# Kernel tuning notes

Hardware: AMD Instinct MI355X
Metric: run time of the kernel (lower is better)

The kernel has to match this reference:

```python
import jax, jax.numpy as jnp
import numpy as np

H = 8              # n_heads
N_PER_GRAPH = 64   # nodes per graph (equal-sized graphs)


def setup_inputs() -> dict:
    key = jax.random.key(0)
    ks = jax.random.split(key, 5)
    total, D = 65536, 512
    x = jax.random.normal(ks[0], (total, D), dtype=jnp.float32)
    batch = jnp.arange(total, dtype=jnp.int64) // N_PER_GRAPH  # sorted graph ids
    s = 1.0 / np.sqrt(D).astype(np.float32)
    # nn.MultiheadAttention packed in-proj (xavier-ish uniform) + zero bias
    in_proj_w = jax.random.uniform(ks[1], (3 * D, D), jnp.float32, -s, s)
    in_proj_b = jnp.zeros((3 * D,), jnp.float32)
    out_proj_w = jax.random.uniform(ks[2], (D, D), jnp.float32, -s, s)
    out_proj_b = jnp.zeros((D,), jnp.float32)
    gate_w = jax.random.uniform(ks[3], (1, D), jnp.float32, -s, s)
    gate_b = jnp.zeros((1,), jnp.float32)
    return {"x": x, "batch": batch, "in_proj_w": in_proj_w, "in_proj_b": in_proj_b,
            "out_proj_w": out_proj_w, "out_proj_b": out_proj_b,
            "gate_w": gate_w, "gate_b": gate_b}


def reference(x, batch, in_proj_w, in_proj_b, out_proj_w, out_proj_b, gate_w, gate_b):
    total, D = x.shape
    G = total // N_PER_GRAPH
    hd = D // H
    xg = x.reshape(G, N_PER_GRAPH, D)                       # [G, N, D]
    # packed qkv projection (torch: x @ in_proj_w.T + in_proj_b)
    qkv = jnp.einsum('gnd,ed->gne', xg, in_proj_w) + in_proj_b
    q, k, v = jnp.split(qkv, 3, axis=-1)
    def to_heads(t):
        return t.reshape(G, N_PER_GRAPH, H, hd).transpose(0, 2, 1, 3)  # [G, H, N, hd]
    q, k, v = to_heads(q), to_heads(k), to_heads(v)
    scores = jnp.einsum('ghnd,ghmd->ghnm', q, k) * (1.0 / np.sqrt(hd))
    attn = jax.nn.softmax(scores, axis=-1)
    ctx = jnp.einsum('ghnm,ghmd->ghnd', attn, v)
    ctx = ctx.transpose(0, 2, 1, 3).reshape(G, N_PER_GRAPH, D)
    attn_out = jnp.einsum('gnd,ed->gne', ctx, out_proj_w) + out_proj_b  # [G, N, D]
    gates = jax.nn.sigmoid(jnp.einsum('gnd,od->gno', attn_out, gate_w) + gate_b)
    return (attn_out * gates).sum(axis=1)                   # [G, D]
```

## Files before the change

### kernel.cpp

```cpp
#include <hip/hip_runtime.h>
#include <stdint.h>


typedef __attribute__((ext_vector_type(8))) short short8;
typedef __attribute__((ext_vector_type(4))) float f32x4;

#define D_ 512

#define WQKV_OFF   0u
#define WO_OFF     1572864u
#define UPART_OFF  2097152u
#define U_OFF      2129920u
#define C0_OFF     2131968u

__device__ __forceinline__ unsigned short f2bf(float f) {
    union { float f; unsigned int u; } t; t.f = f;
    unsigned int u = t.u;
    return (unsigned short)((u + 0x7FFFu + ((u >> 16) & 1u)) >> 16);
}
__device__ __forceinline__ unsigned pack2(float a, float b) {
    return (unsigned)f2bf(a) | ((unsigned)f2bf(b) << 16);
}
__device__ __forceinline__ float blo(unsigned v) {
    union { unsigned u; float f; } t; t.u = v << 16; return t.f;
}
__device__ __forceinline__ float bhi(unsigned v) {
    union { unsigned u; float f; } t; t.u = v & 0xFFFF0000u; return t.f;
}

__global__ __launch_bounds__(256)
void convert_and_u(const float* __restrict__ wqkv, const float* __restrict__ wo,
                   const float* __restrict__ gw,
                   unsigned short* __restrict__ wbf, float* __restrict__ upart) {
    const int b = blockIdx.x;
    const int t = threadIdx.x;
    if (b < 1024) {
        const int i4 = b * 256 + t;
        float4 v;
        if (i4 < 196608) v = *(const float4*)(wqkv + (size_t)i4 * 4);
        else             v = *(const float4*)(wo   + (size_t)(i4 - 196608) * 4);
        uint2 p; p.x = pack2(v.x, v.y); p.y = pack2(v.z, v.w);
        *(uint2*)(wbf + (size_t)i4 * 4) = p;
    } else {
        const int bb = b - 1024;
        float a0 = 0.f, a1 = 0.f;
        #pragma unroll 4
        for (int e = bb * 32; e < bb * 32 + 32; ++e) {
            const float ge = gw[e];
            a0 += wo[(size_t)e * 512 + t]       * ge;
            a1 += wo[(size_t)e * 512 + t + 256] * ge;
        }
        upart[bb * 512 + t] = a0; upart[bb * 512 + t + 256] = a1;
    }
}

__global__ __launch_bounds__(256)
void finalize_u(const float* __restrict__ upart, const float* __restrict__ bo,
                const float* __restrict__ gw, const float* __restrict__ gb,
                float* __restrict__ u, float* __restrict__ c0) {
    const int t = threadIdx.x;
    float s0 = 0.f, s1 = 0.f;
    #pragma unroll
    for (int b = 0; b < 16; ++b) { s0 += upart[b*512 + t]; s1 += upart[b*512 + t + 256]; }
    u[t] = s0; u[t + 256] = s1;
    __shared__ float rb[256];
    rb[t] = bo[t] * gw[t] + bo[t + 256] * gw[t + 256];
    __syncthreads();
    for (int s = 128; s > 0; s >>= 1) { if (t < s) rb[t] += rb[t + s]; __syncthreads(); }
    if (t == 0) c0[0] = rb[0] + gb[0];
}

union U8 { unsigned u[4]; short8 s; };

__global__ __launch_bounds__(512, 2)
void attn_full_kernel(const float* __restrict__ x,
                      const unsigned short* __restrict__ wqkv,
                      const float* __restrict__ bqkv,
                      const unsigned short* __restrict__ wo_bf,
                      const float* __restrict__ bo,
                      const float* __restrict__ u,
                      const float* __restrict__ c0,
                      float* __restrict__ out)
{
    __shared__ unsigned short xs[64][520];
    __shared__ float logitp[8][64];
    __shared__ float gatev[64];
    __shared__ float sgs;

    const int g    = blockIdx.x;
    const int tid  = threadIdx.x;
    const int w    = tid >> 6;
    const int lane = tid & 63;
    const int l15  = lane & 15;
    const int quad = lane >> 4;

    #pragma unroll
    for (int i = 0; i < 16; ++i) {
        int idx = tid + i * 512;
        int row = idx >> 7;
        int c4  = idx & 127;
        float4 v = *(const float4*)(x + ((size_t)(g*64 + row))*512 + c4*4);
        uint2 p; p.x = pack2(v.x, v.y); p.y = pack2(v.z, v.w);
        *(uint2*)(&xs[row][c4*4]) = p;
    }
    __syncthreads();

    const int h = w;

    U8 qA[4][2], kB[4][2];
    #pragma unroll
    for (int dt = 0; dt < 4; ++dt) {
        f32x4 aq[4], ak[4];
        #pragma unroll
        for (int nt = 0; nt < 4; ++nt) {
            aq[nt] = (f32x4){0.f,0.f,0.f,0.f};
            ak[nt] = (f32x4){0.f,0.f,0.f,0.f};
        }
        const unsigned short* wq = wqkv + (size_t)(       h*64 + dt*16 + l15) * 512;
        const unsigned short* wk = wqkv + (size_t)(512 +  h*64 + dt*16 + l15) * 512;
        #pragma unroll 4
        for (int ks = 0; ks < 16; ++ks) {
            const int col = ks*32 + quad*8;
            short8 a0 = *(const short8*)(wq + col);
            short8 a1 = *(const short8*)(wk + col);
            #pragma unroll
            for (int nt = 0; nt < 4; ++nt) {
                short8 b = *(const short8*)(&xs[nt*16 + l15][col]);
                aq[nt] = __builtin_amdgcn_mfma_f32_16x16x32_bf16(a0, b, aq[nt], 0,0,0);
                ak[nt] = __builtin_amdgcn_mfma_f32_16x16x32_bf16(a1, b, ak[nt], 0,0,0);
            }
        }
        float bq[4], bk2[4];
        #pragma unroll
        for (int r = 0; r < 4; ++r) {
            bq[r]  = bqkv[       h*64 + dt*16 + quad*4 + r];
            bk2[r] = bqkv[512 +  h*64 + dt*16 + quad*4 + r];
        }
        const bool take = ((quad >> 1) == (dt & 1));
        const int  ks2  = dt >> 1;
        #pragma unroll
        for (int nt = 0; nt < 4; ++nt) {
            unsigned q01 = pack2(aq[nt][0]+bq[0],  aq[nt][1]+bq[1]);
            unsigned q23 = pack2(aq[nt][2]+bq[2],  aq[nt][3]+bq[3]);
            unsigned k01 = pack2(ak[nt][0]+bk2[0], ak[nt][1]+bk2[1]);
            unsigned k23 = pack2(ak[nt][2]+bk2[2], ak[nt][3]+bk2[3]);
            #pragma unroll
            for (int j = 0; j < 4; ++j) {
                int srcl = ((quad & 1)*2 + (j >> 1))*16 + l15;
                unsigned tq = (unsigned)__shfl((int)((j & 1) ? q23 : q01), srcl);
                unsigned tk = (unsigned)__shfl((int)((j & 1) ? k23 : k01), srcl);
                if (take) { qA[nt][ks2].u[j] = tq; kB[nt][ks2].u[j] = tk; }
            }
        }
    }

    U8 pA[4][2];
    #pragma unroll
    for (int a = 0; a < 4; ++a) {
        f32x4 sc[4];
        #pragma unroll
        for (int b = 0; b < 4; ++b) sc[b] = (f32x4){0.f,0.f,0.f,0.f};
        #pragma unroll
        for (int ks2 = 0; ks2 < 2; ++ks2)
            #pragma unroll
            for (int b = 0; b < 4; ++b)
                sc[b] = __builtin_amdgcn_mfma_f32_16x16x32_bf16(
                            kB[b][ks2].s, qA[a][ks2].s, sc[b], 0,0,0);
        float m0 = -1e30f;
        #pragma unroll
        for (int b = 0; b < 4; ++b)
            #pragma unroll
            for (int r = 0; r < 4; ++r) { sc[b][r] *= 0.125f; m0 = fmaxf(m0, sc[b][r]); }
        m0 = fmaxf(m0, __shfl_xor(m0, 16));
        m0 = fmaxf(m0, __shfl_xor(m0, 32));
        float ssum = 0.f;
        #pragma unroll
        for (int b = 0; b < 4; ++b)
            #pragma unroll
            for (int r = 0; r < 4; ++r) { float e = __expf(sc[b][r] - m0); sc[b][r] = e; ssum += e; }
        ssum += __shfl_xor(ssum, 16);
        ssum += __shfl_xor(ssum, 32);
        float inv = 1.0f / ssum;
        unsigned pp[4][2];
        #pragma unroll
        for (int b = 0; b < 4; ++b) {
            pp[b][0] = pack2(sc[b][0]*inv, sc[b][1]*inv);
            pp[b][1] = pack2(sc[b][2]*inv, sc[b][3]*inv);
        }
        #pragma unroll
        for (int ks2 = 0; ks2 < 2; ++ks2)
            #pragma unroll
            for (int j = 0; j < 4; ++j) {
                int srcl = ((quad & 1)*2 + (j >> 1))*16 + l15;
                unsigned t0 = (unsigned)__shfl((int)pp[ks2*2    ][j & 1], srcl);
                unsigned t1 = (unsigned)__shfl((int)pp[ks2*2 + 1][j & 1], srcl);
                pA[a][ks2].u[j] = (quad >> 1) ? t1 : t0;
            }
    }

    U8 vB[4][2];
    float ym[2][8];
    #pragma unroll
    for (int ks2 = 0; ks2 < 2; ++ks2)
        #pragma unroll
        for (int m = 0; m < 8; ++m) ym[ks2][m] = 0.f;
    #pragma unroll
    for (int dt = 0; dt < 4; ++dt) {
        f32x4 av[4];
        #pragma unroll
        for (int mt = 0; mt < 4; ++mt) av[mt] = (f32x4){0.f,0.f,0.f,0.f};
        const unsigned short* wv = wqkv + (size_t)(1024 + h*64 + dt*16 + l15) * 512;
        #pragma unroll 4
        for (int ks = 0; ks < 16; ++ks) {
            const int col = ks*32 + quad*8;
            short8 a2 = *(const short8*)(wv + col);
            #pragma unroll
            for (int mt = 0; mt < 4; ++mt) {
                short8 b = *(const short8*)(&xs[mt*16 + l15][col]);
                av[mt] = __builtin_amdgcn_mfma_f32_16x16x32_bf16(b, a2, av[mt], 0,0,0);
            }
        }
        const float bv = bqkv[1024 + h*64 + dt*16 + l15];
        unsigned vpk[4][2];
        #pragma unroll
        for (int mt = 0; mt < 4; ++mt) {
            vpk[mt][0] = pack2(av[mt][0]+bv, av[mt][1]+bv);
            vpk[mt][1] = pack2(av[mt][2]+bv, av[mt][3]+bv);
        }
        #pragma unroll
        for (int ks2 = 0; ks2 < 2; ++ks2)
            #pragma unroll
            for (int j = 0; j < 4; ++j) {
                int srcl = ((quad & 1)*2 + (j >> 1))*16 + l15;
                unsigned t0 = (unsigned)__shfl((int)vpk[ks2*2    ][j & 1], srcl);
                unsigned t1 = (unsigned)__shfl((int)vpk[ks2*2 + 1][j & 1], srcl);
                vB[dt][ks2].u[j] = (quad >> 1) ? t1 : t0;
            }
        const float ulv = u[h*64 + dt*16 + l15];
        #pragma unroll
        for (int ks2 = 0; ks2 < 2; ++ks2)
            #pragma unroll
            for (int j = 0; j < 4; ++j) {
                unsigned vv = vB[dt][ks2].u[j];
                ym[ks2][2*j]   += blo(vv) * ulv;
                ym[ks2][2*j+1] += bhi(vv) * ulv;
            }
    }
    #pragma unroll
    for (int ks2 = 0; ks2 < 2; ++ks2)
        #pragma unroll
        for (int m = 0; m < 8; ++m) {
            float v = ym[ks2][m];
            v += __shfl_xor(v, 1); v += __shfl_xor(v, 2);
            v += __shfl_xor(v, 4); v += __shfl_xor(v, 8);
            ym[ks2][m] = v;
        }

    #pragma unroll
    for (int a = 0; a < 4; ++a) {
        float lg = 0.f;
        #pragma unroll
        for (int ks2 = 0; ks2 < 2; ++ks2)
            #pragma unroll
            for (int j = 0; j < 4; ++j) {
                unsigned pv = pA[a][ks2].u[j];
                lg += blo(pv) * ym[ks2][2*j] + bhi(pv) * ym[ks2][2*j+1];
            }
        lg += __shfl_xor(lg, 16);
        lg += __shfl_xor(lg, 32);
        if (quad == 0) logitp[w][a*16 + l15] = lg;
    }
    __syncthreads();

    if (tid < 64) {
        float lg = c0[0];
        #pragma unroll
        for (int ww = 0; ww < 8; ++ww) lg += logitp[ww][tid];
        float gt = 1.0f / (1.0f + __expf(-lg));
        gatev[tid] = gt;
        float s = gt;
        s += __shfl_xor(s, 1);  s += __shfl_xor(s, 2);  s += __shfl_xor(s, 4);
        s += __shfl_xor(s, 8);  s += __shfl_xor(s, 16); s += __shfl_xor(s, 32);
        if (tid == 0) sgs = s;
    }
    __syncthreads();

    float* wctxs = (float*)&xs[0][0];
    {
        float gl[4];
        #pragma unroll
        for (int a = 0; a < 4; ++a) gl[a] = gatev[a*16 + l15];
        float tm[2][8];
        #pragma unroll
        for (int ks2 = 0; ks2 < 2; ++ks2)
            #pragma unroll
            for (int j = 0; j < 4; ++j) {
                float t0 = 0.f, t1 = 0.f;
                #pragma unroll
                for (int a = 0; a < 4; ++a) {
                    unsigned pv = pA[a][ks2].u[j];
                    t0 += blo(pv) * gl[a];
                    t1 += bhi(pv) * gl[a];
                }
                tm[ks2][2*j] = t0; tm[ks2][2*j+1] = t1;
            }
        #pragma unroll
        for (int ks2 = 0; ks2 < 2; ++ks2)
            #pragma unroll
            for (int m = 0; m < 8; ++m) {
                float v = tm[ks2][m];
                v += __shfl_xor(v, 1); v += __shfl_xor(v, 2);
                v += __shfl_xor(v, 4); v += __shfl_xor(v, 8);
                tm[ks2][m] = v;
            }
        #pragma unroll
        for (int dt = 0; dt < 4; ++dt) {
            float s = 0.f;
            #pragma unroll
            for (int ks2 = 0; ks2 < 2; ++ks2)
                #pragma unroll
                for (int j = 0; j < 4; ++j) {
                    unsigned vv = vB[dt][ks2].u[j];
                    s += blo(vv) * tm[ks2][2*j] + bhi(vv) * tm[ks2][2*j+1];
                }
            s += __shfl_xor(s, 16);
            s += __shfl_xor(s, 32);
            if (quad == 0) wctxs[h*64 + dt*16 + l15] = s;
        }
    }
    __syncthreads();

    {
        const unsigned short* wr = wo_bf + (size_t)tid * 512;
        float acc = 0.f;
        #pragma unroll 8
        for (int i = 0; i < 64; ++i) {
            uint4  w4 = *(const uint4*)(wr + i*8);
            float4 ca = *(const float4*)(wctxs + i*8);
            float4 cb = *(const float4*)(wctxs + i*8 + 4);
            acc += blo(w4.x)*ca.x + bhi(w4.x)*ca.y + blo(w4.y)*ca.z + bhi(w4.y)*ca.w
                 + blo(w4.z)*cb.x + bhi(w4.z)*cb.y + blo(w4.w)*cb.z + bhi(w4.w)*cb.w;
        }
        out[(size_t)g*512 + tid] = acc + sgs * bo[tid];
    }
}

extern "C" void kernel_launch(void* const* d_in, const int* in_sizes, int n_in,
                              void* d_out, int out_size, void* d_ws, size_t ws_size,
                              hipStream_t stream) {
    const float* x    = (const float*)d_in[0];
    const float* wqkv = (const float*)d_in[2];
    const float* bqkv = (const float*)d_in[3];
    const float* wo   = (const float*)d_in[4];
    const float* bo   = (const float*)d_in[5];
    const float* gw   = (const float*)d_in[6];
    const float* gb   = (const float*)d_in[7];
    float* out = (float*)d_out;

    char* ws = (char*)d_ws;
    unsigned short* wqkv_bf = (unsigned short*)(ws + WQKV_OFF);
    unsigned short* wo_bf   = (unsigned short*)(ws + WO_OFF);
    float*          upart   = (float*)(ws + UPART_OFF);
    float*          u_ws    = (float*)(ws + U_OFF);
    float*          c0_ws   = (float*)(ws + C0_OFF);

    const int total = in_sizes[0] / D_;
    const int G     = total / 64;

    hipLaunchKernelGGL(convert_and_u, dim3(1040), dim3(256), 0, stream,
                       wqkv, wo, gw, wqkv_bf, upart);
    hipLaunchKernelGGL(finalize_u,    dim3(1),    dim3(256), 0, stream,
                       upart, bo, gw, gb, u_ws, c0_ws);
    hipLaunchKernelGGL(attn_full_kernel, dim3(G), dim3(512), 0, stream,
                       x, wqkv_bf, bqkv, wo_bf, bo, u_ws, c0_ws, out);
}
```

Baseline: 487.1 us.

## Swizzle x tile in LDS, use MFMA for out-proj, merge aux kernels

```diff
diff --git a/kernel.cpp b/kernel.cpp
--- a/kernel.cpp
+++ b/kernel.cpp
@@ -1,4 +1,5 @@
 #include <hip/hip_runtime.h>
+#include <hip/hip_bf16.h>
 #include <stdint.h>
 
 
@@ -10,16 +11,11 @@
 #define WQKV_OFF   0u
 #define WO_OFF     1572864u
 #define UPART_OFF  2097152u
-#define U_OFF      2129920u
 #define C0_OFF     2131968u
 
-__device__ __forceinline__ unsigned short f2bf(float f) {
-    union { float f; unsigned int u; } t; t.f = f;
-    unsigned int u = t.u;
-    return (unsigned short)((u + 0x7FFFu + ((u >> 16) & 1u)) >> 16);
-}
 __device__ __forceinline__ unsigned pack2(float a, float b) {
-    return (unsigned)f2bf(a) | ((unsigned)f2bf(b) << 16);
+    __hip_bfloat162 h = __float22bfloat162_rn(make_float2(a, b));
+    unsigned r; __builtin_memcpy(&r, &h, 4); return r;
 }
 __device__ __forceinline__ float blo(unsigned v) {
     union { unsigned u; float f; } t; t.u = v << 16; return t.f;
@@ -29,9 +25,12 @@
 }
 
 __global__ __launch_bounds__(256)
-void convert_and_u(const float* __restrict__ wqkv, const float* __restrict__ wo,
-                   const float* __restrict__ gw,
-                   unsigned short* __restrict__ wbf, float* __restrict__ upart) {
+void aux_kernel(const float* __restrict__ wqkv, const float* __restrict__ wo,
+                const float* __restrict__ gw, const float* __restrict__ bo,
+                const float* __restrict__ gb,
+                unsigned short* __restrict__ wbf, float* __restrict__ upart,
+                float* __restrict__ c0) {
+    __shared__ float rb[256];
     const int b = blockIdx.x;
     const int t = threadIdx.x;
     if (b < 1024) {
@@ -41,7 +40,7 @@
         else             v = *(const float4*)(wo   + (size_t)(i4 - 196608) * 4);
         uint2 p; p.x = pack2(v.x, v.y); p.y = pack2(v.z, v.w);
         *(uint2*)(wbf + (size_t)i4 * 4) = p;
-    } else {
+    } else if (b < 1040) {
         const int bb = b - 1024;
         float a0 = 0.f, a1 = 0.f;
         #pragma unroll 4
@@ -51,23 +50,12 @@
             a1 += wo[(size_t)e * 512 + t + 256] * ge;
         }
         upart[bb * 512 + t] = a0; upart[bb * 512 + t + 256] = a1;
-    }
-}
-
-__global__ __launch_bounds__(256)
-void finalize_u(const float* __restrict__ upart, const float* __restrict__ bo,
-                const float* __restrict__ gw, const float* __restrict__ gb,
-                float* __restrict__ u, float* __restrict__ c0) {
-    const int t = threadIdx.x;
-    float s0 = 0.f, s1 = 0.f;
-    #pragma unroll
-    for (int b = 0; b < 16; ++b) { s0 += upart[b*512 + t]; s1 += upart[b*512 + t + 256]; }
-    u[t] = s0; u[t + 256] = s1;
-    __shared__ float rb[256];
-    rb[t] = bo[t] * gw[t] + bo[t + 256] * gw[t + 256];
-    __syncthreads();
-    for (int s = 128; s > 0; s >>= 1) { if (t < s) rb[t] += rb[t + s]; __syncthreads(); }
-    if (t == 0) c0[0] = rb[0] + gb[0];
+    } else {
+        rb[t] = bo[t] * gw[t] + bo[t + 256] * gw[t + 256];
+        __syncthreads();
+        for (int s = 128; s > 0; s >>= 1) { if (t < s) rb[t] += rb[t + s]; __syncthreads(); }
+        if (t == 0) c0[0] = rb[0] + gb[0];
+    }
 }
 
 union U8 { unsigned u[4]; short8 s; };
@@ -78,14 +66,15 @@
                       const float* __restrict__ bqkv,
                       const unsigned short* __restrict__ wo_bf,
                       const float* __restrict__ bo,
-                      const float* __restrict__ u,
+                      const float* __restrict__ upart,
                       const float* __restrict__ c0,
                       float* __restrict__ out)
 {
-    __shared__ unsigned short xs[64][520];
-    __shared__ float logitp[8][64];
-    __shared__ float gatev[64];
-    __shared__ float sgs;
+    __shared__ unsigned short xs[64 * 512];
+    float* wctxs  = (float*)xs;
+    float* logitp = (float*)xs + 512;
+    float* gatev  = (float*)xs + 1024;
+    float* sgsp   = (float*)xs + 1088;
 
     const int g    = blockIdx.x;
     const int tid  = threadIdx.x;
@@ -93,15 +82,18 @@
     const int lane = tid & 63;
     const int l15  = lane & 15;
     const int quad = lane >> 4;
+    const int q7   = l15 & 7;
 
     #pragma unroll
     for (int i = 0; i < 16; ++i) {
-        int idx = tid + i * 512;
-        int row = idx >> 7;
-        int c4  = idx & 127;
+        int idx  = tid + i * 512;
+        int row  = idx >> 7;
+        int c4   = idx & 127;
+        int ch   = c4 >> 1;
+        int half = c4 & 1;
         float4 v = *(const float4*)(x + ((size_t)(g*64 + row))*512 + c4*4);
         uint2 p; p.x = pack2(v.x, v.y); p.y = pack2(v.z, v.w);
-        *(uint2*)(&xs[row][c4*4]) = p;
+        *(uint2*)(xs + row*512 + ((ch ^ (row & 7)) << 3) + (half << 2)) = p;
     }
     __syncthreads();
 
@@ -125,7 +117,7 @@
             short8 a1 = *(const short8*)(wk + col);
             #pragma unroll
             for (int nt = 0; nt < 4; ++nt) {
-                short8 b = *(const short8*)(&xs[nt*16 + l15][col]);
+                short8 b = *(const short8*)(xs + (nt*16 + l15)*512 + (((ks*4 + quad) ^ q7) << 3));
                 aq[nt] = __builtin_amdgcn_mfma_f32_16x16x32_bf16(a0, b, aq[nt], 0,0,0);
                 ak[nt] = __builtin_amdgcn_mfma_f32_16x16x32_bf16(a1, b, ak[nt], 0,0,0);
             }
@@ -196,6 +188,15 @@
                 unsigned t1 = (unsigned)__shfl((int)pp[ks2*2 + 1][j & 1], srcl);
                 pA[a][ks2].u[j] = (quad >> 1) ? t1 : t0;
             }
+    }
+
+    float u4[4];
+    #pragma unroll
+    for (int dt = 0; dt < 4; ++dt) {
+        float s = 0.f;
+        #pragma unroll
+        for (int bb = 0; bb < 16; ++bb) s += upart[bb*512 + h*64 + dt*16 + l15];
+        u4[dt] = s;
     }
 
     U8 vB[4][2];
@@ -216,7 +217,7 @@
             short8 a2 = *(const short8*)(wv + col);
             #pragma unroll
             for (int mt = 0; mt < 4; ++mt) {
-                short8 b = *(const short8*)(&xs[mt*16 + l15][col]);
+                short8 b = *(const short8*)(xs + (mt*16 + l15)*512 + (((ks*4 + quad) ^ q7) << 3));
                 av[mt] = __builtin_amdgcn_mfma_f32_16x16x32_bf16(b, a2, av[mt], 0,0,0);
             }
         }
@@ -236,7 +237,7 @@
                 unsigned t1 = (unsigned)__shfl((int)vpk[ks2*2 + 1][j & 1], srcl);
                 vB[dt][ks2].u[j] = (quad >> 1) ? t1 : t0;
             }
-        const float ulv = u[h*64 + dt*16 + l15];
+        const float ulv = u4[dt];
         #pragma unroll
         for (int ks2 = 0; ks2 < 2; ++ks2)
             #pragma unroll
@@ -256,6 +257,8 @@
             ym[ks2][m] = v;
         }
 
+    __syncthreads();
+
     #pragma unroll
     for (int a = 0; a < 4; ++a) {
         float lg = 0.f;
@@ -268,24 +271,23 @@
             }
         lg += __shfl_xor(lg, 16);
         lg += __shfl_xor(lg, 32);
-        if (quad == 0) logitp[w][a*16 + l15] = lg;
+        if (quad == 0) logitp[w*64 + a*16 + l15] = lg;
     }
     __syncthreads();
 
     if (tid < 64) {
         float lg = c0[0];
         #pragma unroll
-        for (int ww = 0; ww < 8; ++ww) lg += logitp[ww][tid];
+        for (int ww = 0; ww < 8; ++ww) lg += logitp[ww*64 + tid];
         float gt = 1.0f / (1.0f + __expf(-lg));
         gatev[tid] = gt;
         float s = gt;
         s += __shfl_xor(s, 1);  s += __shfl_xor(s, 2);  s += __shfl_xor(s, 4);
         s += __shfl_xor(s, 8);  s += __shfl_xor(s, 16); s += __shfl_xor(s, 32);
-        if (tid == 0) sgs = s;
-    }
-    __syncthreads();
-
-    float* wctxs = (float*)&xs[0][0];
+        if (tid == 0) sgsp[0] = s;
+    }
+    __syncthreads();
+
     {
         float gl[4];
         #pragma unroll
@@ -331,17 +333,37 @@
     __syncthreads();
 
     {
-        const unsigned short* wr = wo_bf + (size_t)tid * 512;
-        float acc = 0.f;
-        #pragma unroll 8
-        for (int i = 0; i < 64; ++i) {
-            uint4  w4 = *(const uint4*)(wr + i*8);
-            float4 ca = *(const float4*)(wctxs + i*8);
-            float4 cb = *(const float4*)(wctxs + i*8 + 4);
-            acc += blo(w4.x)*ca.x + bhi(w4.x)*ca.y + blo(w4.y)*ca.z + bhi(w4.y)*ca.w
-                 + blo(w4.z)*cb.x + bhi(w4.z)*cb.y + blo(w4.w)*cb.z + bhi(w4.w)*cb.w;
-        }
-        out[(size_t)g*512 + tid] = acc + sgs * bo[tid];
+        const float sgv = sgsp[0];
+        f32x4 oc[4];
+        #pragma unroll
+        for (int et = 0; et < 4; ++et) oc[et] = (f32x4){0.f,0.f,0.f,0.f};
+        const unsigned short* wr = wo_bf + (size_t)(w*64) * 512;
+        #pragma unroll 4
+        for (int ks = 0; ks < 16; ++ks) {
+            float4 ca = *(const float4*)(wctxs + ks*32 + quad*8);
+            float4 cb = *(const float4*)(wctxs + ks*32 + quad*8 + 4);
+            U8 bf;
+            bf.u[0] = pack2(ca.x, ca.y); bf.u[1] = pack2(ca.z, ca.w);
+            bf.u[2] = pack2(cb.x, cb.y); bf.u[3] = pack2(cb.z, cb.w);
+            #pragma unroll
+            for (int et = 0; et < 4; ++et) {
+                short8 af = *(const short8*)(wr + (size_t)(et*16 + l15)*512 + ks*32 + quad*8);
+                oc[et] = __builtin_amdgcn_mfma_f32_16x16x32_bf16(af, bf.s, oc[et], 0,0,0);
+            }
+        }
+        if (l15 == 0) {
+            #pragma unroll
+            for (int et = 0; et < 4; ++et) {
+                const int e0 = w*64 + et*16 + quad*4;
+                float4 bv = *(const float4*)(bo + e0);
+                float4 ov;
+                ov.x = oc[et][0] + sgv * bv.x;
+                ov.y = oc[et][1] + sgv * bv.y;
+                ov.z = oc[et][2] + sgv * bv.z;
+                ov.w = oc[et][3] + sgv * bv.w;
+                *(float4*)(out + (size_t)g*512 + e0) = ov;
+            }
+        }
     }
 }
 
@@ -361,16 +383,13 @@
     unsigned short* wqkv_bf = (unsigned short*)(ws + WQKV_OFF);
     unsigned short* wo_bf   = (unsigned short*)(ws + WO_OFF);
     float*          upart   = (float*)(ws + UPART_OFF);
-    float*          u_ws    = (float*)(ws + U_OFF);
     float*          c0_ws   = (float*)(ws + C0_OFF);
 
     const int total = in_sizes[0] / D_;
     const int G     = total / 64;
 
-    hipLaunchKernelGGL(convert_and_u, dim3(1040), dim3(256), 0, stream,
-                       wqkv, wo, gw, wqkv_bf, upart);
-    hipLaunchKernelGGL(finalize_u,    dim3(1),    dim3(256), 0, stream,
-                       upart, bo, gw, gb, u_ws, c0_ws);
+    hipLaunchKernelGGL(aux_kernel, dim3(1041), dim3(256), 0, stream,
+                       wqkv, wo, gw, bo, gb, wqkv_bf, upart, c0_ws);
     hipLaunchKernelGGL(attn_full_kernel, dim3(G), dim3(512), 0, stream,
-                       x, wqkv_bf, bqkv, wo_bf, bo, u_ws, c0_ws, out);
-}
+                       x, wqkv_bf, bqkv, wo_bf, bo, upart, c0_ws, out);
+}
```

New measurement: 464.6 us. 1.05x faster.
